# Optimization experiments

Hardware: AMD Instinct MI355X
Metric: run time of the kernel (lower is better)

The kernel has to match this reference:

```python
import jax, jax.numpy as jnp
import numpy as np

NUM_HEADS = 16
HEAD_DIM = 64
KERNEL = 13  # odd
DIM = NUM_HEADS * HEAD_DIM
SCALE = HEAD_DIM ** -0.5


def setup_inputs() -> dict:
    key = jax.random.key(0)
    ks = jax.random.split(key, 6)
    B, L = 4, 4096
    return {
        "x": jax.random.normal(ks[0], (B, L, DIM), jnp.float32),
        "w_qkv": jax.random.normal(ks[1], (DIM, 3 * DIM), jnp.float32) * 0.02,
        "b_qkv": jax.random.normal(ks[2], (3 * DIM,), jnp.float32) * 0.02,
        "rpb": jax.random.normal(ks[3], (NUM_HEADS, 2 * KERNEL - 1), jnp.float32) * 0.02,
        "w_proj": jax.random.normal(ks[4], (DIM, DIM), jnp.float32) * 0.02,
        "b_proj": jax.random.normal(ks[5], (DIM,), jnp.float32) * 0.02,
    }


def _na1d(q, k, v, rpb, kernel_size):
    # q,k,v: [B,H,L,D]; rpb: [H, 2K-1]. dilation == 1.
    L = q.shape[2]
    K = kernel_size
    r = K // 2
    i = jnp.arange(L)
    # neighborhood start, clamped so each query sees exactly K keys (NATTEN semantics)
    ni = jnp.clip(i - r, 0, L - K)                    # [L]
    nbr = ni[:, None] + jnp.arange(K)                 # [L,K] key indices
    k_nb = k[:, :, nbr]                               # [B,H,L,K,D]
    attn = jnp.einsum("bhld,bhlkd->bhlk", q, k_nb)   # windowed QK
    # relative-position-bias start index: bias idx = (key_pos - i) + (K-1)
    pi = ni - i + (K - 1)                             # [L]
    bias = rpb[:, pi[:, None] + jnp.arange(K)]        # [H,L,K]
    attn = jax.nn.softmax(attn + bias[None], axis=-1)
    v_nb = v[:, :, nbr]                               # [B,H,L,K,D]
    return jnp.einsum("bhlk,bhlkd->bhld", attn, v_nb)


def reference(x, w_qkv, b_qkv, rpb, w_proj, b_proj):
    B, L, C = x.shape
    qkv = x @ w_qkv + b_qkv                           # [B,L,3C]
    qkv = qkv.reshape(B, L, 3, NUM_HEADS, HEAD_DIM).transpose(2, 0, 3, 1, 4)
    q, k, v = qkv[0] * SCALE, qkv[1], qkv[2]          # [B,H,L,D]
    out = _na1d(q, k, v, rpb, KERNEL)                 # [B,H,L,D]
    out = out.transpose(0, 2, 1, 3).reshape(B, L, C)
    return out @ w_proj + b_proj
```

## Files before the change

kernel.cpp:

```cpp
#include <hip/hip_runtime.h>

typedef __bf16 bf16x8_t __attribute__((ext_vector_type(8)));
typedef float  f32x4_t  __attribute__((ext_vector_type(4)));
typedef float  floatx4  __attribute__((ext_vector_type(4)));
typedef unsigned short ushortx4 __attribute__((ext_vector_type(4)));

__device__ __forceinline__ float bf2f(unsigned short u) {
    union { unsigned int i; float f; } c; c.i = ((unsigned int)u) << 16; return c.f;
}
__device__ __forceinline__ unsigned short f2bf(float f) {
    union { float f; unsigned int i; } c; c.f = f;
    unsigned int u = c.i;
    u += 0x7fffu + ((u >> 16) & 1u);
    return (unsigned short)(u >> 16);
}
__device__ __forceinline__ void cvt8(uint4 u, floatx4& lo, floatx4& hi) {
    union { unsigned int i; float f; } c;
    c.i = u.x << 16;          lo.x = c.f;
    c.i = u.x & 0xffff0000u;  lo.y = c.f;
    c.i = u.y << 16;          lo.z = c.f;
    c.i = u.y & 0xffff0000u;  lo.w = c.f;
    c.i = u.z << 16;          hi.x = c.f;
    c.i = u.z & 0xffff0000u;  hi.y = c.f;
    c.i = u.w << 16;          hi.z = c.f;
    c.i = u.w & 0xffff0000u;  hi.w = c.f;
}

__device__ __forceinline__ void load_lds16(const unsigned short* g, unsigned short* l) {
    __builtin_amdgcn_global_load_lds(
        (const __attribute__((address_space(1))) unsigned int*)g,
        (__attribute__((address_space(3))) unsigned int*)l, 16, 0, 0);
}

__global__ __launch_bounds__(256) void convert_f32_bf16(
    const float* __restrict__ x, unsigned short* __restrict__ xb)
{
    size_t i = ((size_t)blockIdx.x * 256 + threadIdx.x) * 8;
    floatx4 a = *reinterpret_cast<const floatx4*>(x + i);
    floatx4 b = *reinterpret_cast<const floatx4*>(x + i + 4);
    uint4 o;
    o.x = (unsigned int)f2bf(a.x) | ((unsigned int)f2bf(a.y) << 16);
    o.y = (unsigned int)f2bf(a.z) | ((unsigned int)f2bf(a.w) << 16);
    o.z = (unsigned int)f2bf(b.x) | ((unsigned int)f2bf(b.y) << 16);
    o.w = (unsigned int)f2bf(b.z) | ((unsigned int)f2bf(b.w) << 16);
    *reinterpret_cast<uint4*>(xb + i) = o;
}

__global__ __launch_bounds__(256) void transpose_f32_to_bf16(
    const float* __restrict__ W, unsigned short* __restrict__ Wt,
    int Kdim, int Ndim)
{
    __shared__ float tile[32][33];
    const int n0 = blockIdx.x * 32, k0 = blockIdx.y * 32;
    const int tx = threadIdx.x & 31, ty = threadIdx.x >> 5;
#pragma unroll
    for (int r = 0; r < 4; ++r) {
        int k = ty + r * 8;
        tile[k][tx] = W[(size_t)(k0 + k) * Ndim + n0 + tx];
    }
    __syncthreads();
#pragma unroll
    for (int r = 0; r < 4; ++r) {
        int n = ty + r * 8;
        Wt[(size_t)(n0 + n) * Kdim + k0 + tx] = f2bf(tile[tx][n]);
    }
}

#define TBM 256
#define TBN 256
#define TBK 64

template<bool C_F32>
__global__ __launch_bounds__(512, 2) void gemm_pipe_kernel(
    const unsigned short* __restrict__ A, const unsigned short* __restrict__ Wt,
    const float* __restrict__ bias, void* __restrict__ Cp,
    int N, int K, int lda, int ldc)
{
    __shared__ __align__(16) unsigned short SMEM[65536];

    const int tid  = threadIdx.x;
    const int lane = tid & 63;
    const int wid  = tid >> 6;
    const int wm   = wid >> 2;
    const int wn   = wid & 3;
    const int quad = lane >> 4;
    const int lr   = lane & 15;

    const int gx  = gridDim.x;
    const int cpx = (gx * gridDim.y) >> 3;
    const int bid = blockIdx.y * gx + blockIdx.x;
    const int nid = (bid & 7) * cpx + (bid >> 3);
    const int m0 = (nid / gx) * TBM;
    const int n0 = (nid % gx) * TBN;

    const int s_row8 = tid >> 3;
    const int c_sw   = ((tid & 7) ^ (s_row8 & 7)) * 8;
    const int NT     = K >> 6;

    const unsigned short* Ag = A  + (size_t)(m0 + s_row8) * lda + c_sw;
    const unsigned short* Bg = Wt + (size_t)(n0 + s_row8) * K   + c_sw;

    const int sdst = wid * 512;

    f32x4_t acc[8][4];
#pragma unroll
    for (int i = 0; i < 8; ++i)
#pragma unroll
        for (int j = 0; j < 4; ++j)
            acc[i][j] = (f32x4_t){0.f, 0.f, 0.f, 0.f};

#pragma unroll
    for (int r = 0; r < 4; ++r) {
        load_lds16(Ag + (size_t)(r * 64) * lda, SMEM + r * 4096 + sdst);
        load_lds16(Bg + (size_t)(r * 64) * K,   SMEM + 32768 + r * 4096 + sdst);
    }
    asm volatile("s_waitcnt vmcnt(0)" ::: "memory");
    __builtin_amdgcn_s_barrier();

    const int xk = lr & 7;

    for (int tau = 0; tau < NT; ++tau) {
        const int doff = (tau & 1) * 16384;
        const unsigned short* pa = SMEM + doff;
        const unsigned short* pb = SMEM + 32768 + doff;

        if (tau + 1 < NT) {
            const int noff = ((tau + 1) & 1) * 16384;
            unsigned short* na = SMEM + noff;
            unsigned short* nb = SMEM + 32768 + noff;
            const size_t ko = (size_t)(tau + 1) * TBK;
#pragma unroll
            for (int r = 0; r < 4; ++r) {
                load_lds16(Ag + (size_t)(r * 64) * lda + ko, na + r * 4096 + sdst);
                load_lds16(Bg + (size_t)(r * 64) * K   + ko, nb + r * 4096 + sdst);
            }
        }

        bf16x8_t av[8], bv[4];
#pragma unroll
        for (int j = 0; j < 4; ++j)
            bv[j] = *reinterpret_cast<const bf16x8_t*>(
                pb + (wn * 64 + j * 16 + lr) * 64 + ((quad ^ xk) * 8));
#pragma unroll
        for (int i = 0; i < 8; ++i)
            av[i] = *reinterpret_cast<const bf16x8_t*>(
                pa + (wm * 128 + i * 16 + lr) * 64 + ((quad ^ xk) * 8));
        __builtin_amdgcn_s_setprio(1);
#pragma unroll
        for (int i = 0; i < 8; ++i)
#pragma unroll
            for (int j = 0; j < 4; ++j)
                acc[i][j] = __builtin_amdgcn_mfma_f32_16x16x32_bf16(av[i], bv[j], acc[i][j], 0, 0, 0);
        __builtin_amdgcn_s_setprio(0);

#pragma unroll
        for (int j = 0; j < 4; ++j)
            bv[j] = *reinterpret_cast<const bf16x8_t*>(
                pb + (wn * 64 + j * 16 + lr) * 64 + (((4 + quad) ^ xk) * 8));
#pragma unroll
        for (int i = 0; i < 8; ++i)
            av[i] = *reinterpret_cast<const bf16x8_t*>(
                pa + (wm * 128 + i * 16 + lr) * 64 + (((4 + quad) ^ xk) * 8));
        __builtin_amdgcn_s_setprio(1);
#pragma unroll
        for (int i = 0; i < 8; ++i)
#pragma unroll
            for (int j = 0; j < 4; ++j)
                acc[i][j] = __builtin_amdgcn_mfma_f32_16x16x32_bf16(av[i], bv[j], acc[i][j], 0, 0, 0);
        __builtin_amdgcn_s_setprio(0);

        asm volatile("s_waitcnt vmcnt(0)" ::: "memory");
        __builtin_amdgcn_s_barrier();
    }

    if (C_F32) {
#pragma unroll
        for (int j = 0; j < 4; ++j) {
            int col = n0 + wn * 64 + j * 16 + lr;
            float bj = bias[col];
#pragma unroll
            for (int i = 0; i < 8; ++i) {
                int rbase = m0 + wm * 128 + i * 16 + quad * 4;
#pragma unroll
                for (int r = 0; r < 4; ++r) {
                    float v = acc[i][j][r] + bj;
                    ((float*)Cp)[(size_t)(rbase + r) * ldc + col] = v;
                }
            }
        }
    } else {
        unsigned short* ep = SMEM + wid * 8192;
#pragma unroll
        for (int j = 0; j < 4; ++j) {
            float bj = bias[n0 + wn * 64 + j * 16 + lr];
#pragma unroll
            for (int i = 0; i < 8; ++i) {
#pragma unroll
                for (int r = 0; r < 4; ++r) {
                    int row = i * 16 + quad * 4 + r;
                    int col = j * 16 + lr;
                    int ch  = (col >> 3) ^ (row & 7);
                    ep[row * 64 + ch * 8 + (col & 7)] = f2bf(acc[i][j][r] + bj);
                }
            }
        }
        unsigned short* Cb = (unsigned short*)Cp;
        const int cch = lane & 7;
#pragma unroll
        for (int s = 0; s < 16; ++s) {
            int row = s * 8 + (lane >> 3);
            int ch  = cch ^ (row & 7);
            uint4 v = *reinterpret_cast<const uint4*>(&ep[row * 64 + ch * 8]);
            *reinterpret_cast<uint4*>(
                Cb + (size_t)(m0 + wm * 128 + row) * ldc + n0 + wn * 64 + cch * 8) = v;
        }
    }
}

#define BM 128
#define BN 128
#define BK 32
#define LDT 40

template<bool A_F32, bool C_F32, bool BT>
__global__ __launch_bounds__(256) void gemm_bias_kernel(
    const void* __restrict__ Ap, const void* __restrict__ Wp,
    const float* __restrict__ bias, void* __restrict__ Cp,
    int N, int K, int lda, int ldc)
{
    __shared__ __align__(16) unsigned short As[BM * LDT];
    __shared__ __align__(16) unsigned short Bs[BN * LDT];

    const int tid  = threadIdx.x;
    const int lane = tid & 63;
    const int wid  = tid >> 6;
    const int wm   = wid >> 1;
    const int wn   = wid & 1;
    const int quad = lane >> 4;
    const int lr   = lane & 15;

    const int m0 = blockIdx.y * BM;
    const int n0 = blockIdx.x * BN;

    f32x4_t acc[4][4];
#pragma unroll
    for (int i = 0; i < 4; ++i)
#pragma unroll
        for (int j = 0; j < 4; ++j)
            acc[i][j] = (f32x4_t){0.f, 0.f, 0.f, 0.f};

    for (int k0 = 0; k0 < K; k0 += BK) {
        if (A_F32) {
            const float* A = (const float*)Ap;
#pragma unroll
            for (int it = 0; it < 4; ++it) {
                int q   = tid + it * 256;
                int row = q >> 3;
                int col = (q & 7) * 4;
                floatx4 f = *reinterpret_cast<const floatx4*>(A + (size_t)(m0 + row) * lda + k0 + col);
                ushortx4 s;
                s.x = f2bf(f.x); s.y = f2bf(f.y); s.z = f2bf(f.z); s.w = f2bf(f.w);
                *reinterpret_cast<ushortx4*>(&As[row * LDT + col]) = s;
            }
        } else {
            const unsigned short* A = (const unsigned short*)Ap;
            int a_row = tid >> 2;
            int a_col = (tid & 3) * 8;
#pragma unroll
            for (int r = 0; r < 2; ++r) {
                int row = a_row + r * 64;
                uint4 u = *reinterpret_cast<const uint4*>(A + (size_t)(m0 + row) * lda + k0 + a_col);
                *reinterpret_cast<uint4*>(&As[row * LDT + a_col]) = u;
            }
        }
        if (BT) {
            const unsigned short* Wt = (const unsigned short*)Wp;
            int b_row = tid >> 2;
            int b_col = (tid & 3) * 8;
#pragma unroll
            for (int r = 0; r < 2; ++r) {
                int n = b_row + r * 64;
                uint4 u = *reinterpret_cast<const uint4*>(Wt + (size_t)(n0 + n) * K + k0 + b_col);
                *reinterpret_cast<uint4*>(&Bs[n * LDT + b_col]) = u;
            }
        } else {
            const float* W = (const float*)Wp;
#pragma unroll
            for (int it = 0; it < 4; ++it) {
                int q  = tid + it * 256;
                int kk = q >> 5;
                int nn = (q & 31) * 4;
                floatx4 f = *reinterpret_cast<const floatx4*>(W + (size_t)(k0 + kk) * N + n0 + nn);
                Bs[(nn + 0) * LDT + kk] = f2bf(f.x);
                Bs[(nn + 1) * LDT + kk] = f2bf(f.y);
                Bs[(nn + 2) * LDT + kk] = f2bf(f.z);
                Bs[(nn + 3) * LDT + kk] = f2bf(f.w);
            }
        }
        __syncthreads();

        bf16x8_t av[4], bv[4];
#pragma unroll
        for (int i = 0; i < 4; ++i)
            av[i] = *reinterpret_cast<const bf16x8_t*>(&As[(wm * 64 + i * 16 + lr) * LDT + quad * 8]);
#pragma unroll
        for (int j = 0; j < 4; ++j)
            bv[j] = *reinterpret_cast<const bf16x8_t*>(&Bs[(wn * 64 + j * 16 + lr) * LDT + quad * 8]);

#pragma unroll
        for (int i = 0; i < 4; ++i)
#pragma unroll
            for (int j = 0; j < 4; ++j)
                acc[i][j] = __builtin_amdgcn_mfma_f32_16x16x32_bf16(av[i], bv[j], acc[i][j], 0, 0, 0);

        __syncthreads();
    }

#pragma unroll
    for (int j = 0; j < 4; ++j) {
        int col = n0 + wn * 64 + j * 16 + lr;
        float bj = bias[col];
#pragma unroll
        for (int i = 0; i < 4; ++i) {
            int rbase = m0 + wm * 64 + i * 16 + quad * 4;
#pragma unroll
            for (int r = 0; r < 4; ++r) {
                float v = acc[i][j][r] + bj;
                size_t idx = (size_t)(rbase + r) * ldc + col;
                if (C_F32) ((float*)Cp)[idx] = v;
                else       ((unsigned short*)Cp)[idx] = f2bf(v);
            }
        }
    }
}

#define NA_L 4096
#define NA_K 13
#define NA_H 16
#define NA_D 64
#define NA_SCALE 0.125f
#define TL  64
#define WIN 76

__global__ __launch_bounds__(256) void na1d_tiled_kernel(
    unsigned short* qkv, const float* __restrict__ rpb)
{
    __shared__ __align__(16) unsigned short ks_b[WIN * 64];
    __shared__ __align__(16) unsigned short vs_b[WIN * 64];
    __shared__ __align__(16) unsigned short qs_b[TL * 64];
    __shared__ float wgt[TL][NA_K];

    const int cpx = gridDim.x >> 3;
    const int hb  = blockIdx.x;
    const int bid = (hb & 7) * cpx + (hb >> 3);

    const int h  = bid & 15;
    const int lt = (bid >> 4) & 63;
    const int b  = bid >> 10;
    const int l0 = lt * TL;
    const int rs = l0 - 6;

    const int t = threadIdx.x;
    const size_t rowbase = (size_t)b * NA_L;

    {
        const int qr = t >> 2;
        const int qi = (t & 3) * 2;
        const unsigned short* qsrc = qkv + (rowbase + l0 + qr) * 3072 + h * 64 + qi * 8;
        uint4 q0 = *reinterpret_cast<const uint4*>(qsrc);
        uint4 q1 = *reinterpret_cast<const uint4*>(qsrc + 8);

        const int r0 = t >> 3;
        const int ci = t & 7;
        int g0 = rs + r0;      g0 = g0 < 0 ? 0 : (g0 > NA_L - 1 ? NA_L - 1 : g0);
        int g1 = rs + r0 + 32; g1 = g1 < 0 ? 0 : (g1 > NA_L - 1 ? NA_L - 1 : g1);
        const unsigned short* p0 = qkv + (rowbase + g0) * 3072 + 1024 + h * 64 + ci * 8;
        const unsigned short* p1 = qkv + (rowbase + g1) * 3072 + 1024 + h * 64 + ci * 8;
        uint4 k0 = *reinterpret_cast<const uint4*>(p0);
        uint4 v0 = *reinterpret_cast<const uint4*>(p0 + 1024);
        uint4 k1 = *reinterpret_cast<const uint4*>(p1);
        uint4 v1 = *reinterpret_cast<const uint4*>(p1 + 1024);
        uint4 k2, v2;
        if (t < 96) {
            int g2 = rs + r0 + 64; g2 = g2 < 0 ? 0 : (g2 > NA_L - 1 ? NA_L - 1 : g2);
            const unsigned short* p2 = qkv + (rowbase + g2) * 3072 + 1024 + h * 64 + ci * 8;
            k2 = *reinterpret_cast<const uint4*>(p2);
            v2 = *reinterpret_cast<const uint4*>(p2 + 1024);
        }

        const int qk = qr & 7;
        *reinterpret_cast<uint4*>(qs_b + qr * 64 + (( qi      ^ qk) * 8)) = q0;
        *reinterpret_cast<uint4*>(qs_b + qr * 64 + (((qi + 1) ^ qk) * 8)) = q1;
        const int rk = r0 & 7;
        *reinterpret_cast<uint4*>(ks_b +  r0       * 64 + ((ci ^ rk) * 8)) = k0;
        *reinterpret_cast<uint4*>(vs_b +  r0       * 64 + ((ci ^ rk) * 8)) = v0;
        *reinterpret_cast<uint4*>(ks_b + (r0 + 32) * 64 + ((ci ^ rk) * 8)) = k1;
        *reinterpret_cast<uint4*>(vs_b + (r0 + 32) * 64 + ((ci ^ rk) * 8)) = v1;
        if (t < 96) {
            *reinterpret_cast<uint4*>(ks_b + (r0 + 64) * 64 + ((ci ^ rk) * 8)) = k2;
            *reinterpret_cast<uint4*>(vs_b + (r0 + 64) * 64 + ((ci ^ rk) * 8)) = v2;
        }
    }
    __syncthreads();

    {
        const int l  = t & 63;
        const int jb = (t >> 6) * 4;
        int ig = l0 + l;
        int ni = ig - 6;
        if (ni < 0) ni = 0;
        if (ni > NA_L - NA_K) ni = NA_L - NA_K;
        int rid = ni - rs;
        int pi  = ni - ig + 12;

        int r0r = rid + jb + 0; if (r0r > WIN - 1) r0r = WIN - 1;
        int r1r = rid + jb + 1; if (r1r > WIN - 1) r1r = WIN - 1;
        int r2r = rid + jb + 2; if (r2r > WIN - 1) r2r = WIN - 1;
        int r3r = rid + jb + 3; if (r3r > WIN - 1) r3r = WIN - 1;

        const unsigned short* qrow = qs_b + l * 64;
        const unsigned short* k0p  = ks_b + r0r * 64;
        const unsigned short* k1p  = ks_b + r1r * 64;
        const unsigned short* k2p  = ks_b + r2r * 64;
        const unsigned short* k3p  = ks_b + r3r * 64;
        const int qk = l & 7;
        const int x0 = r0r & 7, x1 = r1r & 7, x2 = r2r & 7, x3 = r3r & 7;

        floatx4 a0 = {0,0,0,0}, a1 = {0,0,0,0}, a2 = {0,0,0,0}, a3 = {0,0,0,0};
#pragma unroll
        for (int c = 0; c < 8; ++c) {
            floatx4 ql, qh, kl, kh;
            cvt8(*reinterpret_cast<const uint4*>(qrow + ((c ^ qk) * 8)), ql, qh);
            cvt8(*reinterpret_cast<const uint4*>(k0p + ((c ^ x0) * 8)), kl, kh);
            a0 += ql * kl; a0 += qh * kh;
            cvt8(*reinterpret_cast<const uint4*>(k1p + ((c ^ x1) * 8)), kl, kh);
            a1 += ql * kl; a1 += qh * kh;
            cvt8(*reinterpret_cast<const uint4*>(k2p + ((c ^ x2) * 8)), kl, kh);
            a2 += ql * kl; a2 += qh * kh;
            cvt8(*reinterpret_cast<const uint4*>(k3p + ((c ^ x3) * 8)), kl, kh);
            a3 += ql * kl; a3 += qh * kh;
        }
        float s0 = (a0.x + a0.y + a0.z + a0.w) * NA_SCALE;
        float s1 = (a1.x + a1.y + a1.z + a1.w) * NA_SCALE;
        float s2 = (a2.x + a2.y + a2.z + a2.w) * NA_SCALE;
        float s3 = (a3.x + a3.y + a3.z + a3.w) * NA_SCALE;
        const float* rp = rpb + h * 25 + pi;
        if (jb + 0 < NA_K) wgt[l][jb + 0] = s0 + rp[jb + 0];
        if (jb + 1 < NA_K) wgt[l][jb + 1] = s1 + rp[jb + 1];
        if (jb + 2 < NA_K) wgt[l][jb + 2] = s2 + rp[jb + 2];
        if (jb + 3 < NA_K) wgt[l][jb + 3] = s3 + rp[jb + 3];
    }
    __syncthreads();

    if (t < TL) {
        float m = -1e30f;
#pragma unroll
        for (int j = 0; j < NA_K; ++j) m = fmaxf(m, wgt[t][j]);
        float sum = 0.f;
#pragma unroll
        for (int j = 0; j < NA_K; ++j) {
            float e = expf(wgt[t][j] - m);
            wgt[t][j] = e;
            sum += e;
        }
        float inv = 1.f / sum;
#pragma unroll
        for (int j = 0; j < NA_K; ++j) wgt[t][j] *= inv;
    }
    __syncthreads();

    {
        const int l  = t & 63;
        const int wv = t >> 6;
        int ig = l0 + l;
        int ni = ig - 6;
        if (ni < 0) ni = 0;
        if (ni > NA_L - NA_K) ni = NA_L - NA_K;
        int rid = ni - rs;
        floatx4 o0 = {0,0,0,0}, o1 = {0,0,0,0}, o2 = {0,0,0,0}, o3 = {0,0,0,0};
#pragma unroll
        for (int j = 0; j < NA_K; ++j) {
            float w = wgt[l][j];
            int r = rid + j;
            int key = r & 7;
            const unsigned short* vrow = vs_b + r * 64;
            floatx4 xl, xh;
            cvt8(*reinterpret_cast<const uint4*>(vrow + (((2 * wv)     ^ key) * 8)), xl, xh);
            o0 += w * xl; o1 += w * xh;
            cvt8(*reinterpret_cast<const uint4*>(vrow + (((2 * wv + 1) ^ key) * 8)), xl, xh);
            o2 += w * xl; o3 += w * xh;
        }
        unsigned short* dst = qkv + (rowbase + ig) * 3072 + h * 64 + wv * 16;
        uint4 p0, p1;
        p0.x = (unsigned int)f2bf(o0.x) | ((unsigned int)f2bf(o0.y) << 16);
        p0.y = (unsigned int)f2bf(o0.z) | ((unsigned int)f2bf(o0.w) << 16);
        p0.z = (unsigned int)f2bf(o1.x) | ((unsigned int)f2bf(o1.y) << 16);
        p0.w = (unsigned int)f2bf(o1.z) | ((unsigned int)f2bf(o1.w) << 16);
        p1.x = (unsigned int)f2bf(o2.x) | ((unsigned int)f2bf(o2.y) << 16);
        p1.y = (unsigned int)f2bf(o2.z) | ((unsigned int)f2bf(o2.w) << 16);
        p1.z = (unsigned int)f2bf(o3.x) | ((unsigned int)f2bf(o3.y) << 16);
        p1.w = (unsigned int)f2bf(o3.z) | ((unsigned int)f2bf(o3.w) << 16);
        *reinterpret_cast<uint4*>(dst)     = p0;
        *reinterpret_cast<uint4*>(dst + 8) = p1;
    }
}

extern "C" void kernel_launch(void* const* d_in, const int* in_sizes, int n_in,
                              void* d_out, int out_size, void* d_ws, size_t ws_size,
                              hipStream_t stream)
{
    const float* x      = (const float*)d_in[0];
    const float* w_qkv  = (const float*)d_in[1];
    const float* b_qkv  = (const float*)d_in[2];
    const float* rpb    = (const float*)d_in[3];
    const float* w_proj = (const float*)d_in[4];
    const float* b_proj = (const float*)d_in[5];
    float* out = (float*)d_out;

    const int M  = 4 * 4096;
    const int K  = 1024;
    const int N1 = 3072;
    const int N2 = 1024;

    unsigned short* qkv = (unsigned short*)d_ws;
    unsigned short* Wt1 = qkv + (size_t)M * N1;
    unsigned short* Wt2 = Wt1 + (size_t)N1 * K;
    unsigned short* xb  = Wt2 + (size_t)N2 * K;
    size_t need_mid  = ((size_t)M * N1 + (size_t)N1 * K + (size_t)N2 * K) * 2;
    size_t need_fast = need_mid + (size_t)M * K * 2;

    const int na_grid = 4 * (NA_L / TL) * NA_H;

    if (ws_size >= need_fast) {
        convert_f32_bf16<<<dim3(M * K / (256 * 8)), 256, 0, stream>>>(x, xb);
        transpose_f32_to_bf16<<<dim3(N1 / 32, K / 32), 256, 0, stream>>>(w_qkv, Wt1, K, N1);
        transpose_f32_to_bf16<<<dim3(N2 / 32, K / 32), 256, 0, stream>>>(w_proj, Wt2, K, N2);
        gemm_pipe_kernel<false><<<dim3(N1 / TBN, M / TBM), 512, 0, stream>>>(
            xb, Wt1, b_qkv, qkv, N1, K, K, N1);
        na1d_tiled_kernel<<<dim3(na_grid), 256, 0, stream>>>(qkv, rpb);
        gemm_pipe_kernel<true><<<dim3(N2 / TBN, M / TBM), 512, 0, stream>>>(
            qkv, Wt2, b_proj, out, N2, K, N1, N2);
    } else if (ws_size >= need_mid) {
        transpose_f32_to_bf16<<<dim3(N1 / 32, K / 32), 256, 0, stream>>>(w_qkv, Wt1, K, N1);
        transpose_f32_to_bf16<<<dim3(N2 / 32, K / 32), 256, 0, stream>>>(w_proj, Wt2, K, N2);
        gemm_bias_kernel<true, false, true><<<dim3(N1 / BN, M / BM), 256, 0, stream>>>(
            x, Wt1, b_qkv, qkv, N1, K, K, N1);
        na1d_tiled_kernel<<<dim3(na_grid), 256, 0, stream>>>(qkv, rpb);
        gemm_bias_kernel<false, true, true><<<dim3(N2 / BN, M / BM), 256, 0, stream>>>(
            qkv, Wt2, b_proj, out, N2, K, N1, N2);
    } else {
        gemm_bias_kernel<true, false, false><<<dim3(N1 / BN, M / BM), 256, 0, stream>>>(
            x, w_qkv, b_qkv, qkv, N1, K, K, N1);
        na1d_tiled_kernel<<<dim3(na_grid), 256, 0, stream>>>(qkv, rpb);
        gemm_bias_kernel<false, true, false><<<dim3(N2 / BN, M / BM), 256, 0, stream>>>(
            qkv, w_proj, b_proj, out, N2, K, N1, N2);
    }
}
```

Before: 335.3 us.

## Replace LDS-tiled neighborhood attention with per-thread register kernel

The shared-memory tiled NA1D kernel is replaced by a kernel that assigns one thread to each (token, head). Each thread holds its query and output accumulators in registers and reads the 13 neighbor K/V rows straight from global memory, relying on cache for reuse across neighbors. This removes the LDS staging, the XOR swizzling and three block-wide barriers. In exchange, K/V traffic through the cache hierarchy goes up and per-thread register use is high (about 130+ floats), which may lower occupancy.

```diff
diff --git a/kernel.cpp b/kernel.cpp
--- a/kernel.cpp
+++ b/kernel.cpp
@@ -337,171 +337,85 @@
 #define NA_L 4096
 #define NA_K 13
 #define NA_H 16
-#define NA_D 64
 #define NA_SCALE 0.125f
-#define TL  64
-#define WIN 76
-
-__global__ __launch_bounds__(256) void na1d_tiled_kernel(
+
+__global__ __launch_bounds__(256) void na1d_reg_kernel(
     unsigned short* qkv, const float* __restrict__ rpb)
 {
-    __shared__ __align__(16) unsigned short ks_b[WIN * 64];
-    __shared__ __align__(16) unsigned short vs_b[WIN * 64];
-    __shared__ __align__(16) unsigned short qs_b[TL * 64];
-    __shared__ float wgt[TL][NA_K];
-
-    const int cpx = gridDim.x >> 3;
-    const int hb  = blockIdx.x;
-    const int bid = (hb & 7) * cpx + (hb >> 3);
-
-    const int h  = bid & 15;
-    const int lt = (bid >> 4) & 63;
-    const int b  = bid >> 10;
-    const int l0 = lt * TL;
-    const int rs = l0 - 6;
-
-    const int t = threadIdx.x;
-    const size_t rowbase = (size_t)b * NA_L;
-
-    {
-        const int qr = t >> 2;
-        const int qi = (t & 3) * 2;
-        const unsigned short* qsrc = qkv + (rowbase + l0 + qr) * 3072 + h * 64 + qi * 8;
-        uint4 q0 = *reinterpret_cast<const uint4*>(qsrc);
-        uint4 q1 = *reinterpret_cast<const uint4*>(qsrc + 8);
-
-        const int r0 = t >> 3;
-        const int ci = t & 7;
-        int g0 = rs + r0;      g0 = g0 < 0 ? 0 : (g0 > NA_L - 1 ? NA_L - 1 : g0);
-        int g1 = rs + r0 + 32; g1 = g1 < 0 ? 0 : (g1 > NA_L - 1 ? NA_L - 1 : g1);
-        const unsigned short* p0 = qkv + (rowbase + g0) * 3072 + 1024 + h * 64 + ci * 8;
-        const unsigned short* p1 = qkv + (rowbase + g1) * 3072 + 1024 + h * 64 + ci * 8;
-        uint4 k0 = *reinterpret_cast<const uint4*>(p0);
-        uint4 v0 = *reinterpret_cast<const uint4*>(p0 + 1024);
-        uint4 k1 = *reinterpret_cast<const uint4*>(p1);
-        uint4 v1 = *reinterpret_cast<const uint4*>(p1 + 1024);
-        uint4 k2, v2;
-        if (t < 96) {
-            int g2 = rs + r0 + 64; g2 = g2 < 0 ? 0 : (g2 > NA_L - 1 ? NA_L - 1 : g2);
-            const unsigned short* p2 = qkv + (rowbase + g2) * 3072 + 1024 + h * 64 + ci * 8;
-            k2 = *reinterpret_cast<const uint4*>(p2);
-            v2 = *reinterpret_cast<const uint4*>(p2 + 1024);
-        }
-
-        const int qk = qr & 7;
-        *reinterpret_cast<uint4*>(qs_b + qr * 64 + (( qi      ^ qk) * 8)) = q0;
-        *reinterpret_cast<uint4*>(qs_b + qr * 64 + (((qi + 1) ^ qk) * 8)) = q1;
-        const int rk = r0 & 7;
-        *reinterpret_cast<uint4*>(ks_b +  r0       * 64 + ((ci ^ rk) * 8)) = k0;
-        *reinterpret_cast<uint4*>(vs_b +  r0       * 64 + ((ci ^ rk) * 8)) = v0;
-        *reinterpret_cast<uint4*>(ks_b + (r0 + 32) * 64 + ((ci ^ rk) * 8)) = k1;
-        *reinterpret_cast<uint4*>(vs_b + (r0 + 32) * 64 + ((ci ^ rk) * 8)) = v1;
-        if (t < 96) {
-            *reinterpret_cast<uint4*>(ks_b + (r0 + 64) * 64 + ((ci ^ rk) * 8)) = k2;
-            *reinterpret_cast<uint4*>(vs_b + (r0 + 64) * 64 + ((ci ^ rk) * 8)) = v2;
-        }
-    }
-    __syncthreads();
-
-    {
-        const int l  = t & 63;
-        const int jb = (t >> 6) * 4;
-        int ig = l0 + l;
-        int ni = ig - 6;
-        if (ni < 0) ni = 0;
-        if (ni > NA_L - NA_K) ni = NA_L - NA_K;
-        int rid = ni - rs;
-        int pi  = ni - ig + 12;
-
-        int r0r = rid + jb + 0; if (r0r > WIN - 1) r0r = WIN - 1;
-        int r1r = rid + jb + 1; if (r1r > WIN - 1) r1r = WIN - 1;
-        int r2r = rid + jb + 2; if (r2r > WIN - 1) r2r = WIN - 1;
-        int r3r = rid + jb + 3; if (r3r > WIN - 1) r3r = WIN - 1;
-
-        const unsigned short* qrow = qs_b + l * 64;
-        const unsigned short* k0p  = ks_b + r0r * 64;
-        const unsigned short* k1p  = ks_b + r1r * 64;
-        const unsigned short* k2p  = ks_b + r2r * 64;
-        const unsigned short* k3p  = ks_b + r3r * 64;
-        const int qk = l & 7;
-        const int x0 = r0r & 7, x1 = r1r & 7, x2 = r2r & 7, x3 = r3r & 7;
-
-        floatx4 a0 = {0,0,0,0}, a1 = {0,0,0,0}, a2 = {0,0,0,0}, a3 = {0,0,0,0};
+    const int t  = blockIdx.x * 256 + threadIdx.x;
+    const int h  = t & 15;
+    const int gl = t >> 4;
+    const int l  = gl & (NA_L - 1);
+
+    int ni = l - 6;
+    if (ni < 0) ni = 0;
+    if (ni > NA_L - NA_K) ni = NA_L - NA_K;
+    const int pi = ni - l + 12;
+
+    const unsigned short* qp    = qkv + (size_t)gl * 3072 + h * 64;
+    const unsigned short* kbase = qkv + ((size_t)(gl - l + ni)) * 3072 + 1024 + h * 64;
+    const float* rp = rpb + h * 25 + pi;
+
+    floatx4 q[16];
+#pragma unroll
+    for (int c = 0; c < 8; ++c) {
+        floatx4 lo, hi;
+        cvt8(*reinterpret_cast<const uint4*>(qp + c * 8), lo, hi);
+        q[2 * c] = lo; q[2 * c + 1] = hi;
+    }
+
+    float w[NA_K];
+    float mx = -1e30f;
+    for (int j = 0; j < NA_K; ++j) {
+        const unsigned short* kp = kbase + (size_t)j * 3072;
+        floatx4 a = {0.f, 0.f, 0.f, 0.f};
 #pragma unroll
         for (int c = 0; c < 8; ++c) {
-            floatx4 ql, qh, kl, kh;
-            cvt8(*reinterpret_cast<const uint4*>(qrow + ((c ^ qk) * 8)), ql, qh);
-            cvt8(*reinterpret_cast<const uint4*>(k0p + ((c ^ x0) * 8)), kl, kh);
-            a0 += ql * kl; a0 += qh * kh;
-            cvt8(*reinterpret_cast<const uint4*>(k1p + ((c ^ x1) * 8)), kl, kh);
-            a1 += ql * kl; a1 += qh * kh;
-            cvt8(*reinterpret_cast<const uint4*>(k2p + ((c ^ x2) * 8)), kl, kh);
-            a2 += ql * kl; a2 += qh * kh;
-            cvt8(*reinterpret_cast<const uint4*>(k3p + ((c ^ x3) * 8)), kl, kh);
-            a3 += ql * kl; a3 += qh * kh;
-        }
-        float s0 = (a0.x + a0.y + a0.z + a0.w) * NA_SCALE;
-        float s1 = (a1.x + a1.y + a1.z + a1.w) * NA_SCALE;
-        float s2 = (a2.x + a2.y + a2.z + a2.w) * NA_SCALE;
-        float s3 = (a3.x + a3.y + a3.z + a3.w) * NA_SCALE;
-        const float* rp = rpb + h * 25 + pi;
-        if (jb + 0 < NA_K) wgt[l][jb + 0] = s0 + rp[jb + 0];
-        if (jb + 1 < NA_K) wgt[l][jb + 1] = s1 + rp[jb + 1];
-        if (jb + 2 < NA_K) wgt[l][jb + 2] = s2 + rp[jb + 2];
-        if (jb + 3 < NA_K) wgt[l][jb + 3] = s3 + rp[jb + 3];
-    }
-    __syncthreads();
-
-    if (t < TL) {
-        float m = -1e30f;
-#pragma unroll
-        for (int j = 0; j < NA_K; ++j) m = fmaxf(m, wgt[t][j]);
-        float sum = 0.f;
-#pragma unroll
-        for (int j = 0; j < NA_K; ++j) {
-            float e = expf(wgt[t][j] - m);
-            wgt[t][j] = e;
-            sum += e;
-        }
-        float inv = 1.f / sum;
-#pragma unroll
-        for (int j = 0; j < NA_K; ++j) wgt[t][j] *= inv;
-    }
-    __syncthreads();
-
-    {
-        const int l  = t & 63;
-        const int wv = t >> 6;
-        int ig = l0 + l;
-        int ni = ig - 6;
-        if (ni < 0) ni = 0;
-        if (ni > NA_L - NA_K) ni = NA_L - NA_K;
-        int rid = ni - rs;
-        floatx4 o0 = {0,0,0,0}, o1 = {0,0,0,0}, o2 = {0,0,0,0}, o3 = {0,0,0,0};
-#pragma unroll
-        for (int j = 0; j < NA_K; ++j) {
-            float w = wgt[l][j];
-            int r = rid + j;
-            int key = r & 7;
-            const unsigned short* vrow = vs_b + r * 64;
-            floatx4 xl, xh;
-            cvt8(*reinterpret_cast<const uint4*>(vrow + (((2 * wv)     ^ key) * 8)), xl, xh);
-            o0 += w * xl; o1 += w * xh;
-            cvt8(*reinterpret_cast<const uint4*>(vrow + (((2 * wv + 1) ^ key) * 8)), xl, xh);
-            o2 += w * xl; o3 += w * xh;
-        }
-        unsigned short* dst = qkv + (rowbase + ig) * 3072 + h * 64 + wv * 16;
-        uint4 p0, p1;
-        p0.x = (unsigned int)f2bf(o0.x) | ((unsigned int)f2bf(o0.y) << 16);
-        p0.y = (unsigned int)f2bf(o0.z) | ((unsigned int)f2bf(o0.w) << 16);
-        p0.z = (unsigned int)f2bf(o1.x) | ((unsigned int)f2bf(o1.y) << 16);
-        p0.w = (unsigned int)f2bf(o1.z) | ((unsigned int)f2bf(o1.w) << 16);
-        p1.x = (unsigned int)f2bf(o2.x) | ((unsigned int)f2bf(o2.y) << 16);
-        p1.y = (unsigned int)f2bf(o2.z) | ((unsigned int)f2bf(o2.w) << 16);
-        p1.z = (unsigned int)f2bf(o3.x) | ((unsigned int)f2bf(o3.y) << 16);
-        p1.w = (unsigned int)f2bf(o3.z) | ((unsigned int)f2bf(o3.w) << 16);
-        *reinterpret_cast<uint4*>(dst)     = p0;
-        *reinterpret_cast<uint4*>(dst + 8) = p1;
+            floatx4 lo, hi;
+            cvt8(*reinterpret_cast<const uint4*>(kp + c * 8), lo, hi);
+            a += q[2 * c] * lo;
+            a += q[2 * c + 1] * hi;
+        }
+        float s = (a.x + a.y + a.z + a.w) * NA_SCALE + rp[j];
+        w[j] = s;
+        mx = fmaxf(mx, s);
+    }
+
+    float sum = 0.f;
+#pragma unroll
+    for (int j = 0; j < NA_K; ++j) {
+        float e = expf(w[j] - mx);
+        w[j] = e;
+        sum += e;
+    }
+    const float inv = 1.f / sum;
+
+    floatx4 o[16];
+#pragma unroll
+    for (int i = 0; i < 16; ++i) o[i] = (floatx4){0.f, 0.f, 0.f, 0.f};
+    const unsigned short* vbase = kbase + 1024;
+    for (int j = 0; j < NA_K; ++j) {
+        const float wj = w[j] * inv;
+        const unsigned short* vp = vbase + (size_t)j * 3072;
+#pragma unroll
+        for (int c = 0; c < 8; ++c) {
+            floatx4 lo, hi;
+            cvt8(*reinterpret_cast<const uint4*>(vp + c * 8), lo, hi);
+            o[2 * c]     += wj * lo;
+            o[2 * c + 1] += wj * hi;
+        }
+    }
+
+    unsigned short* dst = qkv + (size_t)gl * 3072 + h * 64;
+#pragma unroll
+    for (int c = 0; c < 8; ++c) {
+        floatx4 lo = o[2 * c], hi = o[2 * c + 1];
+        uint4 p;
+        p.x = (unsigned int)f2bf(lo.x) | ((unsigned int)f2bf(lo.y) << 16);
+        p.y = (unsigned int)f2bf(lo.z) | ((unsigned int)f2bf(lo.w) << 16);
+        p.z = (unsigned int)f2bf(hi.x) | ((unsigned int)f2bf(hi.y) << 16);
+        p.w = (unsigned int)f2bf(hi.z) | ((unsigned int)f2bf(hi.w) << 16);
+        *reinterpret_cast<uint4*>(dst + c * 8) = p;
     }
 }
 
@@ -529,7 +443,7 @@
     size_t need_mid  = ((size_t)M * N1 + (size_t)N1 * K + (size_t)N2 * K) * 2;
     size_t need_fast = need_mid + (size_t)M * K * 2;
 
-    const int na_grid = 4 * (NA_L / TL) * NA_H;
+    const int na_grid = M * NA_H / 256;
 
     if (ws_size >= need_fast) {
         convert_f32_bf16<<<dim3(M * K / (256 * 8)), 256, 0, stream>>>(x, xb);
@@ -537,7 +451,7 @@
         transpose_f32_to_bf16<<<dim3(N2 / 32, K / 32), 256, 0, stream>>>(w_proj, Wt2, K, N2);
         gemm_pipe_kernel<false><<<dim3(N1 / TBN, M / TBM), 512, 0, stream>>>(
             xb, Wt1, b_qkv, qkv, N1, K, K, N1);
-        na1d_tiled_kernel<<<dim3(na_grid), 256, 0, stream>>>(qkv, rpb);
+        na1d_reg_kernel<<<dim3(na_grid), 256, 0, stream>>>(qkv, rpb);
         gemm_pipe_kernel<true><<<dim3(N2 / TBN, M / TBM), 512, 0, stream>>>(
             qkv, Wt2, b_proj, out, N2, K, N1, N2);
     } else if (ws_size >= need_mid) {
@@ -545,13 +459,13 @@
         transpose_f32_to_bf16<<<dim3(N2 / 32, K / 32), 256, 0, stream>>>(w_proj, Wt2, K, N2);
         gemm_bias_kernel<true, false, true><<<dim3(N1 / BN, M / BM), 256, 0, stream>>>(
             x, Wt1, b_qkv, qkv, N1, K, K, N1);
-        na1d_tiled_kernel<<<dim3(na_grid), 256, 0, stream>>>(qkv, rpb);
+        na1d_reg_kernel<<<dim3(na_grid), 256, 0, stream>>>(qkv, rpb);
         gemm_bias_kernel<false, true, true><<<dim3(N2 / BN, M / BM), 256, 0, stream>>>(
             qkv, Wt2, b_proj, out, N2, K, N1, N2);
     } else {
         gemm_bias_kernel<true, false, false><<<dim3(N1 / BN, M / BM), 256, 0, stream>>>(
             x, w_qkv, b_qkv, qkv, N1, K, K, N1);
-        na1d_tiled_kernel<<<dim3(na_grid), 256, 0, stream>>>(qkv, rpb);
+        na1d_reg_kernel<<<dim3(na_grid), 256, 0, stream>>>(qkv, rpb);
         gemm_bias_kernel<false, true, false><<<dim3(N2 / BN, M / BM), 256, 0, stream>>>(
             qkv, w_proj, b_proj, out, N2, K, N1, N2);
     }
```

Result: slower. 392.8 us (+17.1%).
